# Performance work log

Measured on AMD Instinct MI355X. Metric: run time of the kernel, lower is better.

## Reference

```python
import jax, jax.numpy as jnp
import numpy as np

B, C, H, W = 8, 256, 64, 64
G = min(C // 4, 32)  # 32 groups, as in the torch module
EPS = 1e-6


def setup_inputs() -> dict:
    key = jax.random.key(0)
    ks = jax.random.split(key, 12)
    s = 1.0 / np.sqrt(C)
    inp = {
        "x": jax.random.normal(ks[0], (B, C, H, W), jnp.float32),
        "gn_scale": 1.0 + 0.02 * jax.random.normal(ks[1], (C,), jnp.float32),
        "gn_bias": 0.02 * jax.random.normal(ks[2], (C,), jnp.float32),
        "w_q": s * jax.random.normal(ks[3], (C, C), jnp.float32),
        "b_q": 0.01 * jax.random.normal(ks[4], (C,), jnp.float32),
        "w_k": s * jax.random.normal(ks[5], (C, C), jnp.float32),
        "b_k": 0.01 * jax.random.normal(ks[6], (C,), jnp.float32),
        "w_v": s * jax.random.normal(ks[7], (C, C), jnp.float32),
        "b_v": 0.01 * jax.random.normal(ks[8], (C,), jnp.float32),
        "w_o": s * jax.random.normal(ks[9], (C, C), jnp.float32),
        "b_o": 0.01 * jax.random.normal(ks[10], (C,), jnp.float32),
    }
    return inp


def _group_norm(x, scale, bias):
    b, c, h, w = x.shape
    xg = x.reshape(b, G, c // G, h, w)
    m = jnp.mean(xg, axis=(2, 3, 4), keepdims=True)
    v = jnp.var(xg, axis=(2, 3, 4), keepdims=True)
    xn = ((xg - m) * jax.lax.rsqrt(v + EPS)).reshape(b, c, h, w)
    return xn * scale[None, :, None, None] + bias[None, :, None, None]


def _nin(h, w, b):
    # 1x1 conv: [B,C,H,W] x [out,in] -> [B,out,H,W]
    return jnp.einsum('bchw,oc->bohw', h, w) + b[None, :, None, None]


def reference(x, gn_scale, gn_bias, w_q, b_q, w_k, b_k, w_v, b_v, w_o, b_o):
    b, c, h, w = x.shape
    n = h * w
    hn = _group_norm(x, gn_scale, gn_bias)
    q = _nin(hn, w_q, b_q).reshape(b, c, n)
    k = _nin(hn, w_k, b_k).reshape(b, c, n)
    v = _nin(hn, w_v, b_v).reshape(b, c, n)
    scale = jnp.asarray(c, x.dtype) ** -0.5
    att = jax.nn.softmax(jnp.einsum('bcn,bcm->bnm', q, k) * scale, axis=-1)
    out = jnp.einsum('bnm,bcm->bcn', att, v).reshape(b, c, h, w)
    out = _nin(out, w_o, b_o)
    return (x + out) / jnp.asarray(np.sqrt(2.0), x.dtype)
```

## Files before the change

kernel.cpp:

```cpp
#include <hip/hip_runtime.h>

typedef __attribute__((ext_vector_type(8))) short bf16x8;
typedef __attribute__((ext_vector_type(4))) float f32x4;
typedef unsigned short us;
typedef unsigned char u8;
typedef long i64;

#define MFMA(a, b, c) __builtin_amdgcn_mfma_f32_16x16x32_bf16((a), (b), (c), 0, 0, 0)
#define MFMA8(a, b, c) __builtin_amdgcn_mfma_f32_16x16x32_fp8_fp8((a), (b), (c), 0, 0, 0)

__device__ __forceinline__ us f2bf(float f) {
  union { float f; unsigned int u; } x; x.f = f;
  return (us)((x.u + 0x7FFFu + ((x.u >> 16) & 1u)) >> 16);
}
__device__ __forceinline__ u8 f2fp8(float f) {
  return (u8)(__builtin_amdgcn_cvt_pk_fp8_f32(f, f, 0, false) & 0xFF);
}

__device__ __forceinline__ void glds16(const us* g, us* l) {
  __builtin_amdgcn_global_load_lds(
      (const __attribute__((address_space(1))) unsigned int*)g,
      (__attribute__((address_space(3))) unsigned int*)l, 16, 0, 0);
}

__global__ __launch_bounds__(256) void conv_w(const float* __restrict__ a, const float* __restrict__ b,
                                              const float* __restrict__ c, const float* __restrict__ d,
                                              us* __restrict__ oa, us* __restrict__ ob,
                                              us* __restrict__ oc, us* __restrict__ od) {
  int i = blockIdx.x * 256 + threadIdx.x;
  oa[i] = f2bf(a[i]); ob[i] = f2bf(b[i]); oc[i] = f2bf(c[i]); od[i] = f2bf(d[i]);
}

__global__ __launch_bounds__(256) void gn_kernel(const float* __restrict__ x,
                                                 const float* __restrict__ scale,
                                                 const float* __restrict__ bias,
                                                 us* __restrict__ hnT) {
  int b = blockIdx.y, g = blockIdx.x;
  int tid = threadIdx.x;
  int c0 = g * 8;
  const float* xb = x + (((size_t)b * 256 + c0) << 12);
  float s = 0.f, sq = 0.f;
  for (int j = 0; j < 8; ++j) {
    const float* xc = xb + ((size_t)j << 12);
    for (int n = tid; n < 4096; n += 256) {
      float v = xc[n];
      s += v; sq += v * v;
    }
  }
  for (int off = 32; off; off >>= 1) { s += __shfl_xor(s, off); sq += __shfl_xor(sq, off); }
  __shared__ float red[8];
  int w = tid >> 6, lane = tid & 63;
  if (lane == 0) { red[w] = s; red[4 + w] = sq; }
  __syncthreads();
  s  = red[0] + red[1] + red[2] + red[3];
  sq = red[4] + red[5] + red[6] + red[7];
  float mean = s * (1.f / 32768.f);
  float var  = sq * (1.f / 32768.f) - mean * mean;
  float rstd = rsqrtf(var + 1e-6f);
  float aa[8], bb[8];
  for (int j = 0; j < 8; ++j) {
    float sc = scale[c0 + j] * rstd;
    aa[j] = sc; bb[j] = bias[c0 + j] - mean * sc;
  }
  us* dst = hnT + ((size_t)b << 12) * 256 + c0;
  for (int n = tid; n < 4096; n += 256) {
    union { us u16[8]; uint4 v; } t;
    for (int j = 0; j < 8; ++j) {
      float v = xb[((size_t)j << 12) + n];
      t.u16[j] = f2bf(v * aa[j] + bb[j]);
    }
    *(uint4*)(dst + (size_t)n * 256) = t.v;
  }
}

__global__ __launch_bounds__(256) void proj_nk(const us* __restrict__ hnT,
                                               const us* __restrict__ wq, const us* __restrict__ wk,
                                               const float* __restrict__ bq, const float* __restrict__ bk,
                                               u8* __restrict__ q8, u8* __restrict__ k8) {
  __shared__ us A_s[128 * 64];
  __shared__ us B_s[128 * 64];
  int bx = blockIdx.x, by = blockIdx.y;
  int tid = threadIdx.x, w = tid >> 6, lane = tid & 63;
  int l15 = lane & 15, quad = lane >> 4;
  const us* wsrc; const float* bsrc; u8* dst; int o0;
  if (by < 2) { wsrc = wq; bsrc = bq; dst = q8; o0 = by * 128; }
  else        { wsrc = wk; bsrc = bk; dst = k8; o0 = (by - 2) * 128; }
  size_t R0 = (size_t)bx * 128;
  int wm = (w & 1) * 64, wn = (w >> 1) * 64;
  f32x4 z = {0.f, 0.f, 0.f, 0.f};
  f32x4 acc[4][4] = {{z,z,z,z},{z,z,z,z},{z,z,z,z},{z,z,z,z}};

  for (int kk = 0; kk < 256; kk += 64) {
    __syncthreads();
#pragma unroll
    for (int j = 0; j < 4; ++j) {
      int cidx = j * 256 + tid;
      int row = cidx >> 3, cc = cidx & 7;
      int gch = (cc ^ (row & 7)) * 8;
      glds16(hnT + (R0 + row) * 256 + kk + gch, A_s + cidx * 8);
      glds16(wsrc + (size_t)(o0 + row) * 256 + kk + gch, B_s + cidx * 8);
    }
    __syncthreads();
#pragma unroll
    for (int k2 = 0; k2 < 2; ++k2) {
      int ch = (k2 * 4 + quad) ^ (l15 & 7);
      bf16x8 af[4], bf[4];
#pragma unroll
      for (int i = 0; i < 4; ++i) {
        af[i] = *(const bf16x8*)(A_s + (wm + i * 16 + l15) * 64 + ch * 8);
        bf[i] = *(const bf16x8*)(B_s + (wn + i * 16 + l15) * 64 + ch * 8);
      }
#pragma unroll
      for (int i = 0; i < 4; ++i)
#pragma unroll
        for (int j = 0; j < 4; ++j)
          acc[i][j] = MFMA(af[i], bf[j], acc[i][j]);
    }
  }
#pragma unroll
  for (int j = 0; j < 4; ++j) {
    int o = o0 + wn + j * 16 + l15;
    float bv = bsrc[o];
#pragma unroll
    for (int i = 0; i < 4; ++i)
#pragma unroll
      for (int r = 0; r < 4; ++r)
        dst[(R0 + wm + i * 16 + quad * 4 + r) * 256 + o] = f2fp8(acc[i][j][r] + bv);
  }
}

__global__ __launch_bounds__(256) void proj_cn(const us* __restrict__ A,
                                               const us* __restrict__ Bm,
                                               const float* __restrict__ bias,
                                               const float* __restrict__ x,
                                               float* __restrict__ outf,
                                               u8* __restrict__ out8, int mode) {
  __shared__ us A_s[128 * 64];
  __shared__ us B_s[128 * 64];
  int bx = blockIdx.x, bb = blockIdx.y;
  int mt = bx & 1, ntile = bx >> 1;
  int tid = threadIdx.x, w = tid >> 6, lane = tid & 63;
  int l15 = lane & 15, quad = lane >> 4;
  int R0 = mt * 128;
  size_t NB = (size_t)bb * 4096 + ntile * 128;
  int wm = (w & 1) * 64, wn = (w >> 1) * 64;
  f32x4 z = {0.f, 0.f, 0.f, 0.f};
  f32x4 acc[4][4] = {{z,z,z,z},{z,z,z,z},{z,z,z,z},{z,z,z,z}};

  for (int kk = 0; kk < 256; kk += 64) {
    __syncthreads();
#pragma unroll
    for (int j = 0; j < 4; ++j) {
      int cidx = j * 256 + tid;
      int row = cidx >> 3, cc = cidx & 7;
      int gch = (cc ^ (row & 7)) * 8;
      glds16(A + (size_t)(R0 + row) * 256 + kk + gch, A_s + cidx * 8);
      glds16(Bm + (NB + row) * 256 + kk + gch, B_s + cidx * 8);
    }
    __syncthreads();
#pragma unroll
    for (int k2 = 0; k2 < 2; ++k2) {
      int ch = (k2 * 4 + quad) ^ (l15 & 7);
      bf16x8 af[4], bf[4];
#pragma unroll
      for (int i = 0; i < 4; ++i) {
        af[i] = *(const bf16x8*)(A_s + (wm + i * 16 + l15) * 64 + ch * 8);
        bf[i] = *(const bf16x8*)(B_s + (wn + i * 16 + l15) * 64 + ch * 8);
      }
#pragma unroll
      for (int i = 0; i < 4; ++i)
#pragma unroll
        for (int j = 0; j < 4; ++j)
          acc[i][j] = MFMA(af[i], bf[j], acc[i][j]);
    }
  }
  const float is2 = 0.70710678118654752f;
#pragma unroll
  for (int i = 0; i < 4; ++i)
#pragma unroll
    for (int r = 0; r < 4; ++r) {
      int c = R0 + wm + i * 16 + quad * 4 + r;
      float bv = bias[c];
      size_t base = (((size_t)bb * 256 + c) << 12) + (ntile * 128 + wn);
      if (mode == 0) {
#pragma unroll
        for (int j = 0; j < 4; ++j)
          out8[base + j * 16 + l15] = f2fp8(acc[i][j][r] + bv);
      } else {
#pragma unroll
        for (int j = 0; j < 4; ++j) {
          size_t idx = base + j * 16 + l15;
          outf[idx] = (x[idx] + acc[i][j][r] + bv) * is2;
        }
      }
    }
}

__global__ __launch_bounds__(256) void attn_partial(const u8* __restrict__ q8,
                                                    const u8* __restrict__ k8,
                                                    const u8* __restrict__ v8,
                                                    float* __restrict__ Of,
                                                    us* __restrict__ Ob,
                                                    float* __restrict__ l0,
                                                    float* __restrict__ l1) {
  int b = blockIdx.y, nt = blockIdx.x, h = blockIdx.z;
  int tid = threadIdx.x, w = tid >> 6, lane = tid & 63;
  int l15 = lane & 15, quad = lane >> 4;
  __shared__ u8 kt_s[32 * 256];
  __shared__ u8 v_s[256 * 48];
  __shared__ u8 p_s[4 * 16 * 40];
  const u8* qb = q8 + ((size_t)b << 12) * 256;
  const u8* kb = k8 + ((size_t)b << 12) * 256;
  const u8* vb = v8 + ((size_t)b << 12) * 256;
  int n0 = nt * 64 + w * 16;
  int m_base = h * 2048;
  i64 qf[8];
#pragma unroll
  for (int ks = 0; ks < 8; ++ks)
    qf[ks] = *(const i64*)(qb + (size_t)(n0 + l15) * 256 + ks * 32 + quad * 8);
  f32x4 z = {0.f, 0.f, 0.f, 0.f};
  f32x4 of[16];
#pragma unroll
  for (int i = 0; i < 16; ++i) of[i] = z;
  float lrow[4] = {0.f, 0.f, 0.f, 0.f};

  int km = tid >> 4, kj = tid & 15;
  int km2 = km + 16;
  int ksw = (kj ^ (km & 15)) * 16;
  int vc = tid;

  uint4 kr0 = *(const uint4*)(kb + (size_t)(m_base + km) * 256 + kj * 16);
  uint4 kr1 = *(const uint4*)(kb + (size_t)(m_base + km2) * 256 + kj * 16);
  uint4 vr0 = *(const uint4*)(vb + ((size_t)vc << 12) + m_base);
  uint4 vr1 = *(const uint4*)(vb + ((size_t)vc << 12) + m_base + 16);

  for (int mt = 0; mt < 64; ++mt) {
    __syncthreads();
    *(uint4*)(kt_s + km * 256 + ksw) = kr0;
    *(uint4*)(kt_s + km2 * 256 + ksw) = kr1;
    *(uint4*)(v_s + vc * 48) = vr0;
    *(uint4*)(v_s + vc * 48 + 16) = vr1;
    __syncthreads();
    if (mt < 63) {
      int mn = m_base + (mt + 1) * 32;
      kr0 = *(const uint4*)(kb + (size_t)(mn + km) * 256 + kj * 16);
      kr1 = *(const uint4*)(kb + (size_t)(mn + km2) * 256 + kj * 16);
      vr0 = *(const uint4*)(vb + ((size_t)vc << 12) + mn);
      vr1 = *(const uint4*)(vb + ((size_t)vc << 12) + mn + 16);
    }

    f32x4 s0 = z, s1 = z;
    int r0 = l15, r1 = 16 + l15;
#pragma unroll
    for (int ks = 0; ks < 8; ++ks) {
      int ch = ks * 2 + (quad >> 1), half = (quad & 1) * 8;
      i64 k0 = *(const i64*)(kt_s + r0 * 256 + ((ch ^ (r0 & 15)) * 16) + half);
      i64 k1 = *(const i64*)(kt_s + r1 * 256 + ((ch ^ (r1 & 15)) * 16) + half);
      s0 = MFMA8(qf[ks], k0, s0);
      s1 = MFMA8(qf[ks], k1, s1);
    }

    const float sc = 0.0625f;
    u8* pw = p_s + w * 640;
#pragma unroll
    for (int r = 0; r < 4; ++r) {
      float p0 = __expf(fminf(s0[r] * sc, 5.9f));
      float p1 = __expf(fminf(s1[r] * sc, 5.9f));
      lrow[r] += p0 + p1;
      int pk = __builtin_amdgcn_cvt_pk_fp8_f32(p0, p1, 0, false);
      int n = quad * 4 + r;
      pw[n * 40 + l15]      = (u8)(pk & 0xFF);
      pw[n * 40 + 16 + l15] = (u8)((pk >> 8) & 0xFF);
    }
    i64 pf = *(const i64*)(pw + l15 * 40 + quad * 8);

#pragma unroll
    for (int cs = 0; cs < 16; ++cs) {
      i64 vf = *(const i64*)(v_s + (cs * 16 + l15) * 48 + quad * 8);
      of[cs] = MFMA8(pf, vf, of[cs]);
    }
  }

  size_t obase = ((size_t)b << 12) * 256;
#pragma unroll
  for (int r = 0; r < 4; ++r) {
    int n = n0 + quad * 4 + r;
    float l = lrow[r];
    l += __shfl_xor(l, 1);
    l += __shfl_xor(l, 2);
    l += __shfl_xor(l, 4);
    l += __shfl_xor(l, 8);
    size_t row = obase + (size_t)n * 256;
    if (h == 0) {
      if (l15 == 0) l0[((size_t)b << 12) + n] = l;
#pragma unroll
      for (int cs = 0; cs < 16; ++cs)
        Of[row + cs * 16 + l15] = of[cs][r];
    } else {
      if (l15 == 0) l1[((size_t)b << 12) + n] = l;
#pragma unroll
      for (int cs = 0; cs < 16; ++cs)
        Ob[row + cs * 16 + l15] = f2bf(of[cs][r]);
    }
  }
}

__global__ __launch_bounds__(256) void combine(const float* __restrict__ Of,
                                               const us* __restrict__ Ob,
                                               const float* __restrict__ l0,
                                               const float* __restrict__ l1,
                                               us* __restrict__ attT) {
  int idx = blockIdx.x * 256 + threadIdx.x;
  int row = idx >> 5;
  int c0 = (idx & 31) * 8;
  size_t base = (size_t)row * 256 + c0;
  float inv = 1.f / (l0[row] + l1[row]);
  float4 f0 = *(const float4*)(Of + base);
  float4 f1 = *(const float4*)(Of + base + 4);
  union { us u16[8]; uint4 v; } pb;
  pb.v = *(const uint4*)(Ob + base);
  union { us u16[8]; uint4 v; } t;
  float fo[8] = {f0.x, f0.y, f0.z, f0.w, f1.x, f1.y, f1.z, f1.w};
#pragma unroll
  for (int j = 0; j < 8; ++j) {
    union { unsigned int u; float f; } bu; bu.u = ((unsigned int)pb.u16[j]) << 16;
    t.u16[j] = f2bf((fo[j] + bu.f) * inv);
  }
  *(uint4*)(attT + base) = t.v;
}

extern "C" void kernel_launch(void* const* d_in, const int* in_sizes, int n_in,
                              void* d_out, int out_size, void* d_ws, size_t ws_size,
                              hipStream_t stream) {
  const float* x  = (const float*)d_in[0];
  const float* gs = (const float*)d_in[1];
  const float* gb = (const float*)d_in[2];
  const float* wq = (const float*)d_in[3];
  const float* bq = (const float*)d_in[4];
  const float* wk = (const float*)d_in[5];
  const float* bk = (const float*)d_in[6];
  const float* wv = (const float*)d_in[7];
  const float* bv = (const float*)d_in[8];
  const float* wo = (const float*)d_in[9];
  const float* bo = (const float*)d_in[10];
  float* out = (float*)d_out;

  us* ws = (us*)d_ws;
  const size_t SZ = (size_t)8 * 4096 * 256;
  us* hnT = ws;
  u8* q8  = (u8*)(ws + SZ);
  u8* k8  = q8 + SZ;
  u8* v8  = k8 + SZ;
  us* wqb = (us*)(v8 + SZ);
  us* wkb = wqb + 65536;
  us* wvb = wkb + 65536;
  us* wob = wvb + 65536;
  float* l0 = (float*)(wob + 65536);
  float* l1 = l0 + 32768;
  float* Opart0 = out;
  us* Opart1 = hnT;
  us* attT = (us*)q8;

  conv_w<<<256, 256, 0, stream>>>(wq, wk, wv, wo, wqb, wkb, wvb, wob);
  gn_kernel<<<dim3(32, 8), 256, 0, stream>>>(x, gs, gb, hnT);
  proj_nk<<<dim3(256, 4), 256, 0, stream>>>(hnT, wqb, wkb, bq, bk, q8, k8);
  proj_cn<<<dim3(64, 8), 256, 0, stream>>>(wvb, hnT, bv, nullptr, nullptr, v8, 0);
  attn_partial<<<dim3(64, 8, 2), 256, 0, stream>>>(q8, k8, v8, Opart0, Opart1, l0, l1);
  combine<<<4096, 256, 0, stream>>>(Opart0, Opart1, l0, l1, attT);
  proj_cn<<<dim3(64, 8), 256, 0, stream>>>(wob, attT, bo, x, out, nullptr, 1);
}
```

Baseline: 428.8 us.

## Rewrite attention partial kernel with 32x32x16 fp8 MFMA and larger key tiles

Switches the attention partial kernel from 16x16x32 fp8 MFMAs to 32x32x16 fp8 MFMAs. Each pair of waves now shares a 32-query group and splits the key tile (for S) and the channel range (for PV). The key tile doubles to 64, halving the loop trip count, and the V LDS layout gains an XOR swizzle. This aims to raise MFMA efficiency and cut the LDS fragment loads and sync overhead per FLOP. In exchange it adds an extra block barrier per tile for the P exchange, a shared-memory row-sum reduction, higher register pressure with launch_bounds set to 3, and a strided output store pattern.

```diff
diff --git a/kernel.cpp b/kernel.cpp
--- a/kernel.cpp
+++ b/kernel.cpp
@@ -2,12 +2,13 @@
 
 typedef __attribute__((ext_vector_type(8))) short bf16x8;
 typedef __attribute__((ext_vector_type(4))) float f32x4;
+typedef __attribute__((ext_vector_type(16))) float f32x16;
 typedef unsigned short us;
 typedef unsigned char u8;
 typedef long i64;
 
 #define MFMA(a, b, c) __builtin_amdgcn_mfma_f32_16x16x32_bf16((a), (b), (c), 0, 0, 0)
-#define MFMA8(a, b, c) __builtin_amdgcn_mfma_f32_16x16x32_fp8_fp8((a), (b), (c), 0, 0, 0)
+#define MFMA32(a, b, c) __builtin_amdgcn_mfma_f32_32x32x16_fp8_fp8((a), (b), (c), 0, 0, 0)
 
 __device__ __forceinline__ us f2bf(float f) {
   union { float f; unsigned int u; } x; x.f = f;
@@ -196,111 +197,138 @@
     }
 }
 
-__global__ __launch_bounds__(256) void attn_partial(const u8* __restrict__ q8,
-                                                    const u8* __restrict__ k8,
-                                                    const u8* __restrict__ v8,
-                                                    float* __restrict__ Of,
-                                                    us* __restrict__ Ob,
-                                                    float* __restrict__ l0,
-                                                    float* __restrict__ l1) {
-  int b = blockIdx.y, nt = blockIdx.x, h = blockIdx.z;
+__global__ __launch_bounds__(256, 3) void attn_partial(const u8* __restrict__ q8,
+                                                       const u8* __restrict__ k8,
+                                                       const u8* __restrict__ v8,
+                                                       float* __restrict__ Of,
+                                                       us* __restrict__ Ob,
+                                                       float* __restrict__ l0,
+                                                       float* __restrict__ l1) {
+  int b = blockIdx.y, nt = blockIdx.x, hz = blockIdx.z;
   int tid = threadIdx.x, w = tid >> 6, lane = tid & 63;
-  int l15 = lane & 15, quad = lane >> 4;
-  __shared__ u8 kt_s[32 * 256];
-  __shared__ u8 v_s[256 * 48];
-  __shared__ u8 p_s[4 * 16 * 40];
+  int g = w >> 1, h = w & 1;
+  int l31 = lane & 31, hh = lane >> 5;
+  __shared__ u8 kt_s[64 * 256];
+  __shared__ u8 v_s[256 * 72];
+  __shared__ u8 p_s[2 * 32 * 72];
+  __shared__ float lred[2 * 32];
   const u8* qb = q8 + ((size_t)b << 12) * 256;
   const u8* kb = k8 + ((size_t)b << 12) * 256;
   const u8* vb = v8 + ((size_t)b << 12) * 256;
-  int n0 = nt * 64 + w * 16;
-  int m_base = h * 2048;
-  i64 qf[8];
-#pragma unroll
-  for (int ks = 0; ks < 8; ++ks)
-    qf[ks] = *(const i64*)(qb + (size_t)(n0 + l15) * 256 + ks * 32 + quad * 8);
-  f32x4 z = {0.f, 0.f, 0.f, 0.f};
-  f32x4 of[16];
-#pragma unroll
-  for (int i = 0; i < 16; ++i) of[i] = z;
-  float lrow[4] = {0.f, 0.f, 0.f, 0.f};
-
-  int km = tid >> 4, kj = tid & 15;
-  int km2 = km + 16;
-  int ksw = (kj ^ (km & 15)) * 16;
-  int vc = tid;
-
-  uint4 kr0 = *(const uint4*)(kb + (size_t)(m_base + km) * 256 + kj * 16);
-  uint4 kr1 = *(const uint4*)(kb + (size_t)(m_base + km2) * 256 + kj * 16);
-  uint4 vr0 = *(const uint4*)(vb + ((size_t)vc << 12) + m_base);
-  uint4 vr1 = *(const uint4*)(vb + ((size_t)vc << 12) + m_base + 16);
-
-  for (int mt = 0; mt < 64; ++mt) {
-    __syncthreads();
-    *(uint4*)(kt_s + km * 256 + ksw) = kr0;
-    *(uint4*)(kt_s + km2 * 256 + ksw) = kr1;
-    *(uint4*)(v_s + vc * 48) = vr0;
-    *(uint4*)(v_s + vc * 48 + 16) = vr1;
-    __syncthreads();
-    if (mt < 63) {
-      int mn = m_base + (mt + 1) * 32;
-      kr0 = *(const uint4*)(kb + (size_t)(mn + km) * 256 + kj * 16);
-      kr1 = *(const uint4*)(kb + (size_t)(mn + km2) * 256 + kj * 16);
-      vr0 = *(const uint4*)(vb + ((size_t)vc << 12) + mn);
-      vr1 = *(const uint4*)(vb + ((size_t)vc << 12) + mn + 16);
-    }
-
-    f32x4 s0 = z, s1 = z;
-    int r0 = l15, r1 = 16 + l15;
-#pragma unroll
-    for (int ks = 0; ks < 8; ++ks) {
-      int ch = ks * 2 + (quad >> 1), half = (quad & 1) * 8;
-      i64 k0 = *(const i64*)(kt_s + r0 * 256 + ((ch ^ (r0 & 15)) * 16) + half);
-      i64 k1 = *(const i64*)(kt_s + r1 * 256 + ((ch ^ (r1 & 15)) * 16) + half);
-      s0 = MFMA8(qf[ks], k0, s0);
-      s1 = MFMA8(qf[ks], k1, s1);
+  int m_base = hz * 2048;
+  int qrow = nt * 64 + g * 32 + l31;
+
+  i64 qf[16];
+#pragma unroll
+  for (int seg = 0; seg < 16; ++seg)
+    qf[seg] = *(const i64*)(qb + (size_t)qrow * 256 + seg * 16 + hh * 8);
+
+  f32x16 oacc[4];
+#pragma unroll
+  for (int cb = 0; cb < 4; ++cb)
+#pragma unroll
+    for (int r = 0; r < 16; ++r) oacc[cb][r] = 0.f;
+  float lsum = 0.f;
+
+  int kr_[4], kj_[4], vr_[4], vj_[4];
+#pragma unroll
+  for (int s = 0; s < 4; ++s) {
+    int c1 = s * 256 + tid;
+    kr_[s] = c1 >> 4; kj_[s] = c1 & 15;
+    vr_[s] = c1 >> 2; vj_[s] = c1 & 3;
+  }
+  uint4 krg[4], vrg[4];
+#pragma unroll
+  for (int s = 0; s < 4; ++s) {
+    krg[s] = *(const uint4*)(kb + (size_t)(m_base + kr_[s]) * 256 + kj_[s] * 16);
+    vrg[s] = *(const uint4*)(vb + ((size_t)vr_[s] << 12) + m_base + vj_[s] * 16);
+  }
+
+  u8* pg = p_s + g * (32 * 72);
+  for (int mt = 0; mt < 32; ++mt) {
+    __syncthreads();
+#pragma unroll
+    for (int s = 0; s < 4; ++s) {
+      *(uint4*)(kt_s + kr_[s] * 256 + ((kj_[s] ^ (kr_[s] & 15)) * 16)) = krg[s];
+      *(uint4*)(v_s + vr_[s] * 72 + ((vj_[s] ^ (vr_[s] & 3)) * 16)) = vrg[s];
+    }
+    __syncthreads();
+    if (mt < 31) {
+      int mn = m_base + (mt + 1) * 64;
+#pragma unroll
+      for (int s = 0; s < 4; ++s) {
+        krg[s] = *(const uint4*)(kb + (size_t)(mn + kr_[s]) * 256 + kj_[s] * 16);
+        vrg[s] = *(const uint4*)(vb + ((size_t)vr_[s] << 12) + mn + vj_[s] * 16);
+      }
+    }
+
+    f32x16 sacc;
+#pragma unroll
+    for (int r = 0; r < 16; ++r) sacc[r] = 0.f;
+    int krow = h * 32 + l31;
+    const u8* kbase = kt_s + krow * 256 + hh * 8;
+    int kx = l31 & 15;
+#pragma unroll
+    for (int seg = 0; seg < 16; ++seg) {
+      i64 kf = *(const i64*)(kbase + ((seg ^ kx) * 16));
+      sacc = MFMA32(kf, qf[seg], sacc);
     }
 
     const float sc = 0.0625f;
-    u8* pw = p_s + w * 640;
-#pragma unroll
-    for (int r = 0; r < 4; ++r) {
-      float p0 = __expf(fminf(s0[r] * sc, 5.9f));
-      float p1 = __expf(fminf(s1[r] * sc, 5.9f));
-      lrow[r] += p0 + p1;
-      int pk = __builtin_amdgcn_cvt_pk_fp8_f32(p0, p1, 0, false);
-      int n = quad * 4 + r;
-      pw[n * 40 + l15]      = (u8)(pk & 0xFF);
-      pw[n * 40 + 16 + l15] = (u8)((pk >> 8) & 0xFF);
-    }
-    i64 pf = *(const i64*)(pw + l15 * 40 + quad * 8);
-
-#pragma unroll
-    for (int cs = 0; cs < 16; ++cs) {
-      i64 vf = *(const i64*)(v_s + (cs * 16 + l15) * 48 + quad * 8);
-      of[cs] = MFMA8(pf, vf, of[cs]);
-    }
+    float p[16];
+#pragma unroll
+    for (int r = 0; r < 16; ++r) {
+      p[r] = __expf(fminf(sacc[r] * sc, 5.9f));
+      lsum += p[r];
+    }
+    u8* prow = pg + l31 * 72 + h * 32 + hh * 4;
+#pragma unroll
+    for (int q = 0; q < 4; ++q) {
+      int pk = __builtin_amdgcn_cvt_pk_fp8_f32(p[q * 4 + 0], p[q * 4 + 1], 0, false);
+      pk = __builtin_amdgcn_cvt_pk_fp8_f32(p[q * 4 + 2], p[q * 4 + 3], pk, true);
+      *(int*)(prow + q * 8) = pk;
+    }
+    __syncthreads();
+
+    i64 pf[4];
+    const u8* pbase = pg + l31 * 72 + hh * 8;
+#pragma unroll
+    for (int ms = 0; ms < 4; ++ms)
+      pf[ms] = *(const i64*)(pbase + ms * 16);
+#pragma unroll
+    for (int cb = 0; cb < 4; ++cb) {
+      int c = h * 128 + cb * 32 + l31;
+      const u8* vbase = v_s + c * 72 + hh * 8;
+      int cx = c & 3;
+#pragma unroll
+      for (int ms = 0; ms < 4; ++ms) {
+        i64 vf = *(const i64*)(vbase + ((ms ^ cx) * 16));
+        oacc[cb] = MFMA32(pf[ms], vf, oacc[cb]);
+      }
+    }
+  }
+
+  lsum += __shfl_xor(lsum, 32);
+  __syncthreads();
+  if (h == 0 && hh == 0) lred[g * 32 + l31] = lsum;
+  __syncthreads();
+  if (h == 1 && hh == 0) {
+    float lt = lred[g * 32 + l31] + lsum;
+    int n = nt * 64 + g * 32 + l31;
+    if (hz == 0) l0[((size_t)b << 12) + n] = lt;
+    else         l1[((size_t)b << 12) + n] = lt;
   }
 
   size_t obase = ((size_t)b << 12) * 256;
 #pragma unroll
-  for (int r = 0; r < 4; ++r) {
-    int n = n0 + quad * 4 + r;
-    float l = lrow[r];
-    l += __shfl_xor(l, 1);
-    l += __shfl_xor(l, 2);
-    l += __shfl_xor(l, 4);
-    l += __shfl_xor(l, 8);
-    size_t row = obase + (size_t)n * 256;
-    if (h == 0) {
-      if (l15 == 0) l0[((size_t)b << 12) + n] = l;
-#pragma unroll
-      for (int cs = 0; cs < 16; ++cs)
-        Of[row + cs * 16 + l15] = of[cs][r];
-    } else {
-      if (l15 == 0) l1[((size_t)b << 12) + n] = l;
-#pragma unroll
-      for (int cs = 0; cs < 16; ++cs)
-        Ob[row + cs * 16 + l15] = f2bf(of[cs][r]);
+  for (int cb = 0; cb < 4; ++cb) {
+    int c = h * 128 + cb * 32 + l31;
+#pragma unroll
+    for (int r = 0; r < 16; ++r) {
+      int nl = (r & 3) + 8 * (r >> 2) + 4 * hh;
+      size_t idx = obase + (size_t)(nt * 64 + g * 32 + nl) * 256 + c;
+      if (hz == 0) Of[idx] = oacc[cb][r];
+      else         Ob[idx] = f2bf(oacc[cb][r]);
     }
   }
 }
```

New measurement: 725.4 us. 1.69x slower.
